# Optimization experiments

Measured on AMD Instinct MI355X. Metric: run time of the kernel, lower is better.

## Reference

```python
import jax, jax.numpy as jnp
import numpy as np

N = 65536      # points
C = 256        # channels
K = 16         # knn_samples
L = 4          # num_blocks
EXP = 4        # MLP expansion
EPS = 1e-5


def layer_norm(x, g, b):
    m = jnp.mean(x, axis=-1, keepdims=True)
    v = jnp.var(x, axis=-1, keepdims=True)
    return (x - m) * jax.lax.rsqrt(v + EPS) * g + b


def setup_inputs() -> dict:
    key = jax.random.key(0)
    ks = jax.random.split(key, 16)
    s = lambda fan_in: 1.0 / np.sqrt(fan_in)
    inp = {
        "x": jax.random.normal(ks[0], (N, C), jnp.float32),
        "knn_idx": jax.random.randint(ks[1], (N, K), 0, N, jnp.int32),
        # per-block stacked params (PyTorch Linear stored as [in, out] here)
        "ln1_g": jnp.ones((L, C), jnp.float32),
        "ln1_b": jnp.zeros((L, C), jnp.float32),
        "w_qkv": jax.random.uniform(ks[2], (L, C, 3 * C), jnp.float32, -s(C), s(C)),
        "w_proj": jax.random.uniform(ks[3], (L, C, C), jnp.float32, -s(C), s(C)),
        "b_proj": jax.random.uniform(ks[4], (L, C), jnp.float32, -s(C), s(C)),
        "ln2_g": jnp.ones((L, C), jnp.float32),
        "ln2_b": jnp.zeros((L, C), jnp.float32),
        "w_fc1": jax.random.uniform(ks[5], (L, C, EXP * C), jnp.float32, -s(C), s(C)),
        "b_fc1": jax.random.uniform(ks[6], (L, EXP * C), jnp.float32, -s(C), s(C)),
        "w_fc2": jax.random.uniform(ks[7], (L, EXP * C, C), jnp.float32, -s(EXP * C), s(EXP * C)),
        "b_fc2": jax.random.uniform(ks[8], (L, C), jnp.float32, -s(EXP * C), s(EXP * C)),
    }
    return inp


def reference(x, knn_idx, ln1_g, ln1_b, w_qkv, w_proj, b_proj,
              ln2_g, ln2_b, w_fc1, b_fc1, w_fc2, b_fc2):
    scale = C ** (-0.5)  # head_dim == C (num_heads == 1)
    for i in range(L):
        # --- KNN attention ---
        h = layer_norm(x, ln1_g[i], ln1_b[i])
        qkv = h @ w_qkv[i]                       # [N, 3C], no bias
        q, k, v = jnp.split(qkv, 3, axis=-1)     # each [N, C]
        kk = k[knn_idx]                          # [N, K, C] neighbor gather
        vv = v[knn_idx]                          # [N, K, C]
        scores = jnp.einsum('nc,nkc->nk', q, kk) * scale
        attn = jax.nn.softmax(scores, axis=-1)   # softmax over K neighbors
        out = jnp.einsum('nk,nkc->nc', attn, vv)
        x = x + (out @ w_proj[i] + b_proj[i])
        # --- MLP ---
        h2 = layer_norm(x, ln2_g[i], ln2_b[i])
        h2 = jax.nn.gelu(h2 @ w_fc1[i] + b_fc1[i], approximate=False)
        x = x + (h2 @ w_fc2[i] + b_fc2[i])
    return x
```

## Files before the change

### kernel.cpp

```cpp
#include <hip/hip_runtime.h>

typedef __attribute__((ext_vector_type(4))) float  f32x4;
typedef __attribute__((ext_vector_type(2))) float  f32x2;
typedef __attribute__((ext_vector_type(8))) __bf16 bf16x8;
typedef __attribute__((ext_vector_type(4))) short  s16x4;
typedef __attribute__((ext_vector_type(8))) short  s16x8;
typedef unsigned char uchar;

__device__ __forceinline__ unsigned short f2bf(float f) {
  unsigned u = __builtin_bit_cast(unsigned, f);
  u += 0x7FFFu + ((u >> 16) & 1u);
  return (unsigned short)(u >> 16);
}
__device__ __forceinline__ float b2f(short s) {
  return __builtin_bit_cast(float, (unsigned)((unsigned short)s) << 16);
}
__device__ __forceinline__ uchar f2fp8(float v) {
  return (uchar)(__builtin_amdgcn_cvt_pk_fp8_f32(v, v, 0, false) & 0xFF);
}
__device__ __forceinline__ float gelu_fast(float v) {
  float u = v * (0.7978845608f + 0.0356774081f * v * v);
  float t = __expf(-2.f * fabsf(u));
  float th = (1.f - t) / (1.f + t);
  th = (u >= 0.f) ? th : -th;
  return 0.5f * v * (1.f + th);
}

__device__ __forceinline__ void gload16(const void* g, void* l) {
  __builtin_amdgcn_global_load_lds(
      (const __attribute__((address_space(1))) void*)g,
      (__attribute__((address_space(3))) void*)l, 16, 0, 0);
}

__global__ __launch_bounds__(256) void wcast(const float* __restrict__ W,
                                             short* __restrict__ WT,
                                             int In, int Out) {
  int i = blockIdx.x * 256 + threadIdx.x;
  int lay = blockIdx.y;
  if (i >= In * Out) return;
  const float* w = W + (size_t)lay * In * Out;
  short* wt = WT + (size_t)lay * In * Out;
  int ii = i % In, oo = i / In;
  wt[(size_t)oo * In + ii] = (short)f2bf(w[(size_t)ii * Out + oo]);
}

__global__ __launch_bounds__(256) void ln_k(const float* __restrict__ x,
                                            const float* __restrict__ g,
                                            const float* __restrict__ b,
                                            short* __restrict__ out) {
  int row = blockIdx.x * 4 + (threadIdx.x >> 6);
  int l = threadIdx.x & 63;
  const float4 v = *(const float4*)(x + (size_t)row * 256 + l * 4);
  float s  = v.x + v.y + v.z + v.w;
  float ss = v.x * v.x + v.y * v.y + v.z * v.z + v.w * v.w;
#pragma unroll
  for (int o = 32; o >= 1; o >>= 1) {
    s  += __shfl_xor(s, o);
    ss += __shfl_xor(ss, o);
  }
  float mean = s * (1.0f / 256.0f);
  float var  = ss * (1.0f / 256.0f) - mean * mean;
  float rstd = rsqrtf(var + 1e-5f);
  const float4 gg = *(const float4*)(g + l * 4);
  const float4 bb = *(const float4*)(b + l * 4);
  s16x4 o4;
  o4[0] = (short)f2bf((v.x - mean) * rstd * gg.x + bb.x);
  o4[1] = (short)f2bf((v.y - mean) * rstd * gg.y + bb.y);
  o4[2] = (short)f2bf((v.z - mean) * rstd * gg.z + bb.z);
  o4[3] = (short)f2bf((v.w - mean) * rstd * gg.w + bb.w);
  *(s16x4*)(out + (size_t)row * 256 + l * 4) = o4;
}

__global__ __launch_bounds__(256) void attn_k(const short* __restrict__ q_,
                                              const uchar* __restrict__ k8,
                                              const uchar* __restrict__ v8,
                                              const int* __restrict__ knn,
                                              short* __restrict__ out) {
  int n = blockIdx.x * 4 + (threadIdx.x >> 6);
  int l = threadIdx.x & 63;
  int j = l & 15, g = l >> 4;
  int idxj = knn[(size_t)n * 16 + j];
  const short* qp = q_ + (size_t)n * 256 + g * 64;
  const uchar* kp = k8 + (size_t)idxj * 256 + g * 64;
  float partial = 0.f;
#pragma unroll
  for (int t = 0; t < 4; ++t) {
    int4 kv = *(const int4*)(kp + t * 16);
    s16x8 q0 = *(const s16x8*)(qp + t * 16);
    s16x8 q1 = *(const s16x8*)(qp + t * 16 + 8);
    f32x2 a;
    a = __builtin_amdgcn_cvt_pk_f32_fp8(kv.x, false);
    partial += a[0] * b2f(q0[0]) + a[1] * b2f(q0[1]);
    a = __builtin_amdgcn_cvt_pk_f32_fp8(kv.x, true);
    partial += a[0] * b2f(q0[2]) + a[1] * b2f(q0[3]);
    a = __builtin_amdgcn_cvt_pk_f32_fp8(kv.y, false);
    partial += a[0] * b2f(q0[4]) + a[1] * b2f(q0[5]);
    a = __builtin_amdgcn_cvt_pk_f32_fp8(kv.y, true);
    partial += a[0] * b2f(q0[6]) + a[1] * b2f(q0[7]);
    a = __builtin_amdgcn_cvt_pk_f32_fp8(kv.z, false);
    partial += a[0] * b2f(q1[0]) + a[1] * b2f(q1[1]);
    a = __builtin_amdgcn_cvt_pk_f32_fp8(kv.z, true);
    partial += a[0] * b2f(q1[2]) + a[1] * b2f(q1[3]);
    a = __builtin_amdgcn_cvt_pk_f32_fp8(kv.w, false);
    partial += a[0] * b2f(q1[4]) + a[1] * b2f(q1[5]);
    a = __builtin_amdgcn_cvt_pk_f32_fp8(kv.w, true);
    partial += a[0] * b2f(q1[6]) + a[1] * b2f(q1[7]);
  }
  partial += __shfl_xor(partial, 16);
  partial += __shfl_xor(partial, 32);
  float score = partial * 0.0625f;
  float mx = score;
#pragma unroll
  for (int o = 1; o < 16; o <<= 1) mx = fmaxf(mx, __shfl_xor(mx, o));
  float e = __expf(score - mx);
  float sum = e;
#pragma unroll
  for (int o = 1; o < 16; o <<= 1) sum += __shfl_xor(sum, o);
  float attn = e / sum;
  float4 o4 = {0.f, 0.f, 0.f, 0.f};
#pragma unroll
  for (int jj = 0; jj < 16; ++jj) {
    float aj = __shfl(attn, jj);
    int   ij = __shfl(idxj, jj);
    int vv = *(const int*)(v8 + (size_t)ij * 256 + l * 4);
    f32x2 lo = __builtin_amdgcn_cvt_pk_f32_fp8(vv, false);
    f32x2 hi = __builtin_amdgcn_cvt_pk_f32_fp8(vv, true);
    o4.x += aj * lo[0];
    o4.y += aj * lo[1];
    o4.z += aj * hi[0];
    o4.w += aj * hi[1];
  }
  s16x4 ob;
  ob[0] = (short)f2bf(o4.x);
  ob[1] = (short)f2bf(o4.y);
  ob[2] = (short)f2bf(o4.z);
  ob[3] = (short)f2bf(o4.w);
  *(s16x4*)(out + (size_t)n * 256 + l * 4) = ob;
}

template <int EPI, int KD>
__global__ __launch_bounds__(256) void gemm_k(
    const short* __restrict__ A, const short* __restrict__ BT,
    const float* __restrict__ bias, const float* __restrict__ resid,
    short* __restrict__ outb, float* __restrict__ outf,
    uchar* __restrict__ k8, uchar* __restrict__ v8, int Nout, int gx) {
  __shared__ __align__(16) char pool[36864];
  short* lA = (short*)pool;
  short* lB = (short*)(pool + 16384);
  const int tid = threadIdx.x;
  const int l = tid & 63, w = tid >> 6;
  const int nwg = gridDim.x;
  const int bid = blockIdx.x;
  const int swz = (bid & 7) * (nwg >> 3) + (bid >> 3);
  const int m0 = (swz / gx) << 7, n0 = (swz % gx) << 7;
  const int wm = w >> 1, wn = w & 1;

  f32x4 acc[4][4];
#pragma unroll
  for (int i = 0; i < 4; ++i)
#pragma unroll
    for (int jj = 0; jj < 4; ++jj) acc[i][jj] = f32x4{0.f, 0.f, 0.f, 0.f};

  const int srow = (w << 3) + (l >> 3);
  const int scol = (((l & 7) << 3)) ^ ((srow & 7) << 3);
  const short* gA = A + (size_t)(m0 + srow) * KD + scol;
  const short* gB = BT + (size_t)(n0 + srow) * KD + scol;

  for (int kt = 0; kt < KD; kt += 64) {
#pragma unroll
    for (int it = 0; it < 4; ++it) {
      gload16(gA + (size_t)(it * 32) * KD + kt, &lA[(it * 32 + w * 8) * 64]);
      gload16(gB + (size_t)(it * 32) * KD + kt, &lB[(it * 32 + w * 8) * 64]);
    }
    __syncthreads();
#pragma unroll
    for (int kc = 0; kc < 2; ++kc) {
      bf16x8 aF[4], bF[4];
#pragma unroll
      for (int f = 0; f < 4; ++f) {
        int r = wm * 64 + f * 16 + (l & 15);
        int ce = (kc * 32 + ((l >> 4) << 3)) ^ ((r & 7) << 3);
        aF[f] = *(const bf16x8*)(lA + r * 64 + ce);
      }
#pragma unroll
      for (int f = 0; f < 4; ++f) {
        int r = wn * 64 + f * 16 + (l & 15);
        int ce = (kc * 32 + ((l >> 4) << 3)) ^ ((r & 7) << 3);
        bF[f] = *(const bf16x8*)(lB + r * 64 + ce);
      }
#pragma unroll
      for (int mf = 0; mf < 4; ++mf)
#pragma unroll
        for (int nf = 0; nf < 4; ++nf)
          acc[mf][nf] = __builtin_amdgcn_mfma_f32_16x16x32_bf16(
              aF[mf], bF[nf], acc[mf][nf], 0, 0, 0);
    }
    __syncthreads();
  }

  const int lr = (l >> 4) << 2, lc = l & 15;
  if (EPI == 1) {
#pragma unroll
    for (int mf = 0; mf < 4; ++mf) {
#pragma unroll
      for (int nf = 0; nf < 4; ++nf) {
#pragma unroll
        for (int jj = 0; jj < 4; ++jj) {
          int row = m0 + wm * 64 + mf * 16 + lr + jj;
          int col = n0 + wn * 64 + nf * 16 + lc;
          float v = acc[mf][nf][jj] + bias[col] + resid[(size_t)row * 256 + col];
          outf[(size_t)row * 256 + col] = v;
        }
      }
    }
    return;
  }

  short* myL = (short*)(pool + w * 9216);
#pragma unroll
  for (int mf = 0; mf < 4; ++mf) {
#pragma unroll
    for (int nf = 0; nf < 4; ++nf) {
#pragma unroll
      for (int jj = 0; jj < 4; ++jj) {
        int rl = mf * 16 + lr + jj;
        int cl = nf * 16 + lc;
        float v = acc[mf][nf][jj];
        if (EPI == 2) v = gelu_fast(v + bias[n0 + wn * 64 + cl]);
        myL[rl * 72 + cl] = (short)f2bf(v);
      }
    }
  }
#pragma unroll
  for (int it = 0; it < 8; ++it) {
    int rl = it * 8 + (l >> 3);
    int cl = (l & 7) * 8;
    s16x8 vv = *(const s16x8*)(myL + rl * 72 + cl);
    int rowg = m0 + wm * 64 + rl;
    int colg = n0 + wn * 64 + cl;
    if (EPI == 2) {
      *(s16x8*)(outb + (size_t)rowg * Nout + colg) = vv;
    } else {
      if (colg < 256) {
        *(s16x8*)(outb + (size_t)rowg * 256 + colg) = vv;
      } else {
        unsigned w0 = __builtin_amdgcn_cvt_pk_fp8_f32(b2f(vv[0]), b2f(vv[1]), 0, false);
        w0 = __builtin_amdgcn_cvt_pk_fp8_f32(b2f(vv[2]), b2f(vv[3]), w0, true);
        unsigned w1 = __builtin_amdgcn_cvt_pk_fp8_f32(b2f(vv[4]), b2f(vv[5]), 0, false);
        w1 = __builtin_amdgcn_cvt_pk_fp8_f32(b2f(vv[6]), b2f(vv[7]), w1, true);
        int2 pk = make_int2((int)w0, (int)w1);
        uchar* dst = (colg < 512) ? (k8 + (size_t)rowg * 256 + (colg - 256))
                                  : (v8 + (size_t)rowg * 256 + (colg - 512));
        *(int2*)dst = pk;
      }
    }
  }
}

extern "C" void kernel_launch(void* const* d_in, const int* in_sizes, int n_in,
                              void* d_out, int out_size, void* d_ws, size_t ws_size,
                              hipStream_t stream) {
  const float* in_x   = (const float*)d_in[0];
  const int*   knn    = (const int*)d_in[1];
  const float* ln1_g  = (const float*)d_in[2];
  const float* ln1_b  = (const float*)d_in[3];
  const float* w_qkv  = (const float*)d_in[4];
  const float* w_proj = (const float*)d_in[5];
  const float* b_proj = (const float*)d_in[6];
  const float* ln2_g  = (const float*)d_in[7];
  const float* ln2_b  = (const float*)d_in[8];
  const float* w_fc1  = (const float*)d_in[9];
  const float* b_fc1  = (const float*)d_in[10];
  const float* w_fc2  = (const float*)d_in[11];
  const float* b_fc2  = (const float*)d_in[12];

  char* ws = (char*)d_ws;
  float* x    = (float*)(ws);
  short* act  = (short*)(ws + 67108864);
  short* big  = (short*)(ws + 100663296);
  short* q_bf = big;
  uchar* k8   = (uchar*)(ws + 134217728);
  uchar* v8   = (uchar*)(ws + 150994944);
  short* wT   = (short*)(ws + 234881024);
  short* wqkvT  = wT;
  short* wprojT = wT + 786432;
  short* wfc1T  = wT + 1048576;
  short* wfc2T  = wT + 2097152;

  wcast<<<dim3(768, 4), 256, 0, stream>>>(w_qkv, wqkvT, 256, 768);
  wcast<<<dim3(256, 4), 256, 0, stream>>>(w_proj, wprojT, 256, 256);
  wcast<<<dim3(1024, 4), 256, 0, stream>>>(w_fc1, wfc1T, 256, 1024);
  wcast<<<dim3(1024, 4), 256, 0, stream>>>(w_fc2, wfc2T, 1024, 256);

  for (int i = 0; i < 4; ++i) {
    const float* xin = (i == 0) ? in_x : x;
    ln_k<<<16384, 256, 0, stream>>>(xin, ln1_g + i * 256, ln1_b + i * 256, act);
    gemm_k<3, 256><<<3072, 256, 0, stream>>>(
        act, wqkvT + (size_t)i * 196608, nullptr, nullptr, q_bf, nullptr,
        k8, v8, 768, 6);
    attn_k<<<16384, 256, 0, stream>>>(q_bf, k8, v8, knn, act);
    gemm_k<1, 256><<<1024, 256, 0, stream>>>(
        act, wprojT + (size_t)i * 65536, b_proj + i * 256, xin, nullptr, x,
        nullptr, nullptr, 256, 2);
    ln_k<<<16384, 256, 0, stream>>>(x, ln2_g + i * 256, ln2_b + i * 256, act);
    gemm_k<2, 256><<<4096, 256, 0, stream>>>(
        act, wfc1T + (size_t)i * 262144, b_fc1 + i * 1024, nullptr, big, nullptr,
        nullptr, nullptr, 1024, 8);
    gemm_k<1, 1024><<<1024, 256, 0, stream>>>(
        big, wfc2T + (size_t)i * 262144, b_fc2 + i * 256, x, nullptr,
        (i == 3) ? (float*)d_out : x, nullptr, nullptr, 256, 2);
  }
}
```

Measured before the change: 1.268 ms.

## Quantize MLP hidden activations and fc2 weights to FP8 for fc2 GEMM

The fc1 epilogue now writes GELU outputs as scaled FP8 (×16) instead of bf16. fc2 weights are cast to FP8 (×64). A new FP8 MFMA GEMM kernel computes fc2 and rescales by 1/1024 before adding bias and the residual. This halves the bytes of the large hidden activation tensor and uses the faster FP8 matrix path, at the cost of extra quantization error in the MLP output.

New measurement: 1.248 ms. No clear change (-1.5%).

```diff
diff --git a/kernel.cpp b/kernel.cpp
--- a/kernel.cpp
+++ b/kernel.cpp
@@ -42,6 +42,16 @@
   short* wt = WT + (size_t)lay * In * Out;
   int ii = i % In, oo = i / In;
   wt[(size_t)oo * In + ii] = (short)f2bf(w[(size_t)ii * Out + oo]);
+}
+
+__global__ __launch_bounds__(256) void wcast8(const float* __restrict__ W,
+                                              uchar* __restrict__ WT8) {
+  int i = blockIdx.x * 256 + threadIdx.x;
+  int lay = blockIdx.y;
+  const float* w = W + (size_t)lay * 262144;
+  uchar* wt = WT8 + (size_t)lay * 262144;
+  int ii = i % 1024, oo = i / 1024;
+  wt[(size_t)oo * 1024 + ii] = f2fp8(64.f * w[(size_t)ii * 256 + oo]);
 }
 
 __global__ __launch_bounds__(256) void ln_k(const float* __restrict__ x,
@@ -239,7 +249,11 @@
     int rowg = m0 + wm * 64 + rl;
     int colg = n0 + wn * 64 + cl;
     if (EPI == 2) {
-      *(s16x8*)(outb + (size_t)rowg * Nout + colg) = vv;
+      unsigned w0 = __builtin_amdgcn_cvt_pk_fp8_f32(16.f * b2f(vv[0]), 16.f * b2f(vv[1]), 0, false);
+      w0 = __builtin_amdgcn_cvt_pk_fp8_f32(16.f * b2f(vv[2]), 16.f * b2f(vv[3]), w0, true);
+      unsigned w1 = __builtin_amdgcn_cvt_pk_fp8_f32(16.f * b2f(vv[4]), 16.f * b2f(vv[5]), 0, false);
+      w1 = __builtin_amdgcn_cvt_pk_fp8_f32(16.f * b2f(vv[6]), 16.f * b2f(vv[7]), w1, true);
+      *(int2*)(k8 + (size_t)rowg * Nout + colg) = make_int2((int)w0, (int)w1);
     } else {
       if (colg < 256) {
         *(s16x8*)(outb + (size_t)rowg * 256 + colg) = vv;
@@ -252,6 +266,80 @@
         uchar* dst = (colg < 512) ? (k8 + (size_t)rowg * 256 + (colg - 256))
                                   : (v8 + (size_t)rowg * 256 + (colg - 512));
         *(int2*)dst = pk;
+      }
+    }
+  }
+}
+
+__global__ __launch_bounds__(256) void gemm_fp8(
+    const uchar* __restrict__ A8, const uchar* __restrict__ B8,
+    const float* __restrict__ bias, const float* __restrict__ resid,
+    float* __restrict__ outf) {
+  __shared__ __align__(16) uchar lA8[8192];
+  __shared__ __align__(16) uchar lB8[8192];
+  const int tid = threadIdx.x;
+  const int l = tid & 63, w = tid >> 6;
+  const int nwg = gridDim.x;
+  const int bid = blockIdx.x;
+  const int swz = (bid & 7) * (nwg >> 3) + (bid >> 3);
+  const int m0 = (swz >> 1) << 7, n0 = (swz & 1) << 7;
+  const int wm = w >> 1, wn = w & 1;
+
+  f32x4 acc[4][4];
+#pragma unroll
+  for (int i = 0; i < 4; ++i)
+#pragma unroll
+    for (int jj = 0; jj < 4; ++jj) acc[i][jj] = f32x4{0.f, 0.f, 0.f, 0.f};
+
+  const int sr = (w << 4) + (l >> 2);
+  const int sc = ((l & 3) << 4) ^ ((sr & 3) << 4);
+  const uchar* gA = A8 + (size_t)(m0 + sr) * 1024 + sc;
+  const uchar* gB = B8 + (size_t)(n0 + sr) * 1024 + sc;
+
+  for (int kt = 0; kt < 1024; kt += 64) {
+#pragma unroll
+    for (int it = 0; it < 2; ++it) {
+      gload16(gA + (size_t)(it * 64) * 1024 + kt, &lA8[(it * 64 + w * 16) * 64]);
+      gload16(gB + (size_t)(it * 64) * 1024 + kt, &lB8[(it * 64 + w * 16) * 64]);
+    }
+    __syncthreads();
+#pragma unroll
+    for (int kc = 0; kc < 2; ++kc) {
+      long aF[4], bF[4];
+#pragma unroll
+      for (int f = 0; f < 4; ++f) {
+        int r = wm * 64 + f * 16 + (l & 15);
+        int cs = (kc * 32 + ((l >> 4) << 3)) ^ ((r & 3) << 4);
+        aF[f] = *(const long*)(lA8 + r * 64 + cs);
+      }
+#pragma unroll
+      for (int f = 0; f < 4; ++f) {
+        int r = wn * 64 + f * 16 + (l & 15);
+        int cs = (kc * 32 + ((l >> 4) << 3)) ^ ((r & 3) << 4);
+        bF[f] = *(const long*)(lB8 + r * 64 + cs);
+      }
+#pragma unroll
+      for (int mf = 0; mf < 4; ++mf)
+#pragma unroll
+        for (int nf = 0; nf < 4; ++nf)
+          acc[mf][nf] = __builtin_amdgcn_mfma_f32_16x16x32_fp8_fp8(
+              aF[mf], bF[nf], acc[mf][nf], 0, 0, 0);
+    }
+    __syncthreads();
+  }
+
+  const int lr = (l >> 4) << 2, lc = l & 15;
+#pragma unroll
+  for (int mf = 0; mf < 4; ++mf) {
+#pragma unroll
+    for (int nf = 0; nf < 4; ++nf) {
+#pragma unroll
+      for (int jj = 0; jj < 4; ++jj) {
+        int row = m0 + wm * 64 + mf * 16 + lr + jj;
+        int col = n0 + wn * 64 + nf * 16 + lc;
+        float v = acc[mf][nf][jj] * (1.0f / 1024.0f) + bias[col] +
+                  resid[(size_t)row * 256 + col];
+        outf[(size_t)row * 256 + col] = v;
       }
     }
   }
@@ -277,20 +365,20 @@
   char* ws = (char*)d_ws;
   float* x    = (float*)(ws);
   short* act  = (short*)(ws + 67108864);
-  short* big  = (short*)(ws + 100663296);
-  short* q_bf = big;
-  uchar* k8   = (uchar*)(ws + 134217728);
-  uchar* v8   = (uchar*)(ws + 150994944);
+  uchar* big8 = (uchar*)(ws + 100663296);
+  short* q_bf = (short*)(ws + 167772160);
+  uchar* k8   = (uchar*)(ws + 201326592);
+  uchar* v8   = (uchar*)(ws + 218103808);
   short* wT   = (short*)(ws + 234881024);
   short* wqkvT  = wT;
   short* wprojT = wT + 786432;
   short* wfc1T  = wT + 1048576;
-  short* wfc2T  = wT + 2097152;
+  uchar* wfc2T8 = (uchar*)(wT + 2097152);
 
   wcast<<<dim3(768, 4), 256, 0, stream>>>(w_qkv, wqkvT, 256, 768);
   wcast<<<dim3(256, 4), 256, 0, stream>>>(w_proj, wprojT, 256, 256);
   wcast<<<dim3(1024, 4), 256, 0, stream>>>(w_fc1, wfc1T, 256, 1024);
-  wcast<<<dim3(1024, 4), 256, 0, stream>>>(w_fc2, wfc2T, 1024, 256);
+  wcast8<<<dim3(1024, 4), 256, 0, stream>>>(w_fc2, wfc2T8);
 
   for (int i = 0; i < 4; ++i) {
     const float* xin = (i == 0) ? in_x : x;
@@ -304,10 +392,10 @@
         nullptr, nullptr, 256, 2);
     ln_k<<<16384, 256, 0, stream>>>(x, ln2_g + i * 256, ln2_b + i * 256, act);
     gemm_k<2, 256><<<4096, 256, 0, stream>>>(
-        act, wfc1T + (size_t)i * 262144, b_fc1 + i * 1024, nullptr, big, nullptr,
-        nullptr, nullptr, 1024, 8);
-    gemm_k<1, 1024><<<1024, 256, 0, stream>>>(
-        big, wfc2T + (size_t)i * 262144, b_fc2 + i * 256, x, nullptr,
-        (i == 3) ? (float*)d_out : x, nullptr, nullptr, 256, 2);
-  }
-}
+        act, wfc1T + (size_t)i * 262144, b_fc1 + i * 1024, nullptr, nullptr,
+        nullptr, big8, nullptr, 1024, 8);
+    gemm_fp8<<<1024, 256, 0, stream>>>(
+        big8, wfc2T8 + (size_t)i * 262144, b_fc2 + i * 256, x,
+        (i == 3) ? (float*)d_out : x);
+  }
+}
```

## Fuse MLP fc1+GELU+fc2 into single kernel keeping hidden activations on-chip

Applied to the files above, without the earlier changes.

Replaces the separate fc1 (with GELU epilogue) and fc2 GEMM launches with one kernel. Each workgroup takes 64 rows, computes the 1024-wide hidden layer in 128-column chunks, applies GELU into per-wave LDS, and accumulates fc2 directly in registers. This removes the round trip of the N×1024 bf16 hidden tensor through global memory. In exchange, weight fragments are read straight from global/L2 without LDS staging, and the fc2 accumulators raise register pressure, which can hurt occupancy.

After: 3.632 ms. +186.5%, slower.

```diff
diff --git a/kernel.cpp b/kernel.cpp
--- a/kernel.cpp
+++ b/kernel.cpp
@@ -14,9 +14,6 @@
 }
 __device__ __forceinline__ float b2f(short s) {
   return __builtin_bit_cast(float, (unsigned)((unsigned short)s) << 16);
-}
-__device__ __forceinline__ uchar f2fp8(float v) {
-  return (uchar)(__builtin_amdgcn_cvt_pk_fp8_f32(v, v, 0, false) & 0xFF);
 }
 __device__ __forceinline__ float gelu_fast(float v) {
   float u = v * (0.7978845608f + 0.0356774081f * v * v);
@@ -225,9 +222,7 @@
       for (int jj = 0; jj < 4; ++jj) {
         int rl = mf * 16 + lr + jj;
         int cl = nf * 16 + lc;
-        float v = acc[mf][nf][jj];
-        if (EPI == 2) v = gelu_fast(v + bias[n0 + wn * 64 + cl]);
-        myL[rl * 72 + cl] = (short)f2bf(v);
+        myL[rl * 72 + cl] = (short)f2bf(acc[mf][nf][jj]);
       }
     }
   }
@@ -238,21 +233,102 @@
     s16x8 vv = *(const s16x8*)(myL + rl * 72 + cl);
     int rowg = m0 + wm * 64 + rl;
     int colg = n0 + wn * 64 + cl;
-    if (EPI == 2) {
-      *(s16x8*)(outb + (size_t)rowg * Nout + colg) = vv;
+    if (colg < 256) {
+      *(s16x8*)(outb + (size_t)rowg * 256 + colg) = vv;
     } else {
-      if (colg < 256) {
-        *(s16x8*)(outb + (size_t)rowg * 256 + colg) = vv;
-      } else {
-        unsigned w0 = __builtin_amdgcn_cvt_pk_fp8_f32(b2f(vv[0]), b2f(vv[1]), 0, false);
-        w0 = __builtin_amdgcn_cvt_pk_fp8_f32(b2f(vv[2]), b2f(vv[3]), w0, true);
-        unsigned w1 = __builtin_amdgcn_cvt_pk_fp8_f32(b2f(vv[4]), b2f(vv[5]), 0, false);
-        w1 = __builtin_amdgcn_cvt_pk_fp8_f32(b2f(vv[6]), b2f(vv[7]), w1, true);
-        int2 pk = make_int2((int)w0, (int)w1);
-        uchar* dst = (colg < 512) ? (k8 + (size_t)rowg * 256 + (colg - 256))
-                                  : (v8 + (size_t)rowg * 256 + (colg - 512));
-        *(int2*)dst = pk;
-      }
+      unsigned w0 = __builtin_amdgcn_cvt_pk_fp8_f32(b2f(vv[0]), b2f(vv[1]), 0, false);
+      w0 = __builtin_amdgcn_cvt_pk_fp8_f32(b2f(vv[2]), b2f(vv[3]), w0, true);
+      unsigned w1 = __builtin_amdgcn_cvt_pk_fp8_f32(b2f(vv[4]), b2f(vv[5]), 0, false);
+      w1 = __builtin_amdgcn_cvt_pk_fp8_f32(b2f(vv[6]), b2f(vv[7]), w1, true);
+      int2 pk = make_int2((int)w0, (int)w1);
+      uchar* dst = (colg < 512) ? (k8 + (size_t)rowg * 256 + (colg - 256))
+                                : (v8 + (size_t)rowg * 256 + (colg - 512));
+      *(int2*)dst = pk;
+    }
+  }
+}
+
+__global__ __launch_bounds__(256) void mlp_k(
+    const short* __restrict__ act, const short* __restrict__ w1T,
+    const float* __restrict__ b1, const short* __restrict__ w2T,
+    const float* __restrict__ b2, const float* __restrict__ resid,
+    float* __restrict__ xout) {
+  __shared__ __align__(16) short lact[64 * 256];
+  __shared__ __align__(16) short la1[4][16 * 128];
+  const int tid = threadIdx.x;
+  const int l = tid & 63, w = tid >> 6;
+  const int nwg = gridDim.x;
+  const int bid = blockIdx.x;
+  const int swz = (bid & 7) * (nwg >> 3) + (bid >> 3);
+  const int m0 = swz << 6;
+
+  {
+    const int sr = w * 2 + (l >> 5);
+    const int sc = ((l & 31) << 3) ^ ((sr & 7) << 3);
+    const short* gA = act + (size_t)(m0 + sr) * 256 + sc;
+#pragma unroll
+    for (int it = 0; it < 8; ++it)
+      gload16(gA + (size_t)(it * 8) * 256, &lact[(it * 8 + w * 2) * 256]);
+  }
+  __syncthreads();
+
+  f32x4 acc2[16];
+#pragma unroll
+  for (int i = 0; i < 16; ++i) acc2[i] = f32x4{0.f, 0.f, 0.f, 0.f};
+
+  const int arow = w * 16 + (l & 15);
+  const int rxor = (l & 7) << 3;
+  const int lrr = ((l >> 4) << 2);
+
+  for (int nc = 0; nc < 8; ++nc) {
+    f32x4 acc1[8];
+#pragma unroll
+    for (int i = 0; i < 8; ++i) acc1[i] = f32x4{0.f, 0.f, 0.f, 0.f};
+#pragma unroll
+    for (int kc = 0; kc < 8; ++kc) {
+      int ce = (kc * 32 + ((l >> 4) << 3)) ^ rxor;
+      bf16x8 aF = *(const bf16x8*)(lact + arow * 256 + ce);
+      int wcol = kc * 32 + ((l >> 4) << 3);
+#pragma unroll
+      for (int nf = 0; nf < 8; ++nf) {
+        int wrow = nc * 128 + nf * 16 + (l & 15);
+        bf16x8 bF = *(const bf16x8*)(w1T + (size_t)wrow * 256 + wcol);
+        acc1[nf] = __builtin_amdgcn_mfma_f32_16x16x32_bf16(aF, bF, acc1[nf], 0, 0, 0);
+      }
+    }
+#pragma unroll
+    for (int nf = 0; nf < 8; ++nf) {
+#pragma unroll
+      for (int j = 0; j < 4; ++j) {
+        int colc = nf * 16 + (l & 15);
+        float v = gelu_fast(acc1[nf][j] + b1[nc * 128 + colc]);
+        int rr = lrr + j;
+        la1[w][rr * 128 + (colc ^ ((rr & 7) << 3))] = (short)f2bf(v);
+      }
+    }
+#pragma unroll
+    for (int kc = 0; kc < 4; ++kc) {
+      int rr = l & 15;
+      int ce = (kc * 32 + ((l >> 4) << 3)) ^ ((rr & 7) << 3);
+      bf16x8 aF = *(const bf16x8*)(&la1[w][rr * 128 + ce]);
+      int kcol = nc * 128 + kc * 32 + ((l >> 4) << 3);
+#pragma unroll
+      for (int nf = 0; nf < 16; ++nf) {
+        int orow = nf * 16 + (l & 15);
+        bf16x8 bF = *(const bf16x8*)(w2T + (size_t)orow * 1024 + kcol);
+        acc2[nf] = __builtin_amdgcn_mfma_f32_16x16x32_bf16(aF, bF, acc2[nf], 0, 0, 0);
+      }
+    }
+  }
+
+#pragma unroll
+  for (int nf = 0; nf < 16; ++nf) {
+#pragma unroll
+    for (int j = 0; j < 4; ++j) {
+      int row = m0 + w * 16 + lrr + j;
+      int col = nf * 16 + (l & 15);
+      float v = acc2[nf][j] + b2[col] + resid[(size_t)row * 256 + col];
+      xout[(size_t)row * 256 + col] = v;
     }
   }
 }
@@ -277,11 +353,10 @@
   char* ws = (char*)d_ws;
   float* x    = (float*)(ws);
   short* act  = (short*)(ws + 67108864);
-  short* big  = (short*)(ws + 100663296);
-  short* q_bf = big;
+  short* q_bf = (short*)(ws + 100663296);
   uchar* k8   = (uchar*)(ws + 134217728);
   uchar* v8   = (uchar*)(ws + 150994944);
-  short* wT   = (short*)(ws + 234881024);
+  short* wT   = (short*)(ws + 167772160);
   short* wqkvT  = wT;
   short* wprojT = wT + 786432;
   short* wfc1T  = wT + 1048576;
@@ -303,11 +378,9 @@
         act, wprojT + (size_t)i * 65536, b_proj + i * 256, xin, nullptr, x,
         nullptr, nullptr, 256, 2);
     ln_k<<<16384, 256, 0, stream>>>(x, ln2_g + i * 256, ln2_b + i * 256, act);
-    gemm_k<2, 256><<<4096, 256, 0, stream>>>(
-        act, wfc1T + (size_t)i * 262144, b_fc1 + i * 1024, nullptr, big, nullptr,
-        nullptr, nullptr, 1024, 8);
-    gemm_k<1, 1024><<<1024, 256, 0, stream>>>(
-        big, wfc2T + (size_t)i * 262144, b_fc2 + i * 256, x, nullptr,
-        (i == 3) ? (float*)d_out : x, nullptr, nullptr, 256, 2);
-  }
-}
+    mlp_k<<<1024, 256, 0, stream>>>(
+        act, wfc1T + (size_t)i * 262144, b_fc1 + i * 1024,
+        wfc2T + (size_t)i * 262144, b_fc2 + i * 256, x,
+        (i == 3) ? (float*)d_out : x);
+  }
+}
```

## Keep residual stream in bf16 and use sigmoid GELU approximation

Applied to the files above, without the earlier changes.

Stores the running residual x as bf16 instead of fp32, so layer norms and residual-add epilogues read and write half the bytes; an initial kernel casts the input to bf16 and the last block writes fp32 output. GELU in the fc1 epilogue is replaced by the cheaper x*sigmoid(1.702x) form. This cuts memory traffic and epilogue ALU work but accumulates rounding error in the residual across blocks and loosens GELU accuracy.

New measurement: 1.084 ms. 14.5% less time.

```diff
diff --git a/kernel.cpp b/kernel.cpp
--- a/kernel.cpp
+++ b/kernel.cpp
@@ -15,21 +15,27 @@
 __device__ __forceinline__ float b2f(short s) {
   return __builtin_bit_cast(float, (unsigned)((unsigned short)s) << 16);
 }
-__device__ __forceinline__ uchar f2fp8(float v) {
-  return (uchar)(__builtin_amdgcn_cvt_pk_fp8_f32(v, v, 0, false) & 0xFF);
-}
-__device__ __forceinline__ float gelu_fast(float v) {
-  float u = v * (0.7978845608f + 0.0356774081f * v * v);
-  float t = __expf(-2.f * fabsf(u));
-  float th = (1.f - t) / (1.f + t);
-  th = (u >= 0.f) ? th : -th;
-  return 0.5f * v * (1.f + th);
+__device__ __forceinline__ float gelu_sig(float v) {
+  float t = __expf(-1.702f * v);
+  return v * __builtin_amdgcn_rcpf(1.f + t);
 }
 
 __device__ __forceinline__ void gload16(const void* g, void* l) {
   __builtin_amdgcn_global_load_lds(
       (const __attribute__((address_space(1))) void*)g,
       (__attribute__((address_space(3))) void*)l, 16, 0, 0);
+}
+
+__global__ __launch_bounds__(256) void x2bf(const float* __restrict__ x,
+                                            short* __restrict__ xb) {
+  int i = blockIdx.x * 256 + threadIdx.x;
+  float4 v = *(const float4*)(x + (size_t)i * 4);
+  s16x4 o;
+  o[0] = (short)f2bf(v.x);
+  o[1] = (short)f2bf(v.y);
+  o[2] = (short)f2bf(v.z);
+  o[3] = (short)f2bf(v.w);
+  *(s16x4*)(xb + (size_t)i * 4) = o;
 }
 
 __global__ __launch_bounds__(256) void wcast(const float* __restrict__ W,
@@ -44,15 +50,16 @@
   wt[(size_t)oo * In + ii] = (short)f2bf(w[(size_t)ii * Out + oo]);
 }
 
-__global__ __launch_bounds__(256) void ln_k(const float* __restrict__ x,
+__global__ __launch_bounds__(256) void ln_k(const short* __restrict__ xb,
                                             const float* __restrict__ g,
                                             const float* __restrict__ b,
                                             short* __restrict__ out) {
   int row = blockIdx.x * 4 + (threadIdx.x >> 6);
   int l = threadIdx.x & 63;
-  const float4 v = *(const float4*)(x + (size_t)row * 256 + l * 4);
-  float s  = v.x + v.y + v.z + v.w;
-  float ss = v.x * v.x + v.y * v.y + v.z * v.z + v.w * v.w;
+  const s16x4 vb = *(const s16x4*)(xb + (size_t)row * 256 + l * 4);
+  float v0 = b2f(vb[0]), v1 = b2f(vb[1]), v2 = b2f(vb[2]), v3 = b2f(vb[3]);
+  float s  = v0 + v1 + v2 + v3;
+  float ss = v0 * v0 + v1 * v1 + v2 * v2 + v3 * v3;
 #pragma unroll
   for (int o = 32; o >= 1; o >>= 1) {
     s  += __shfl_xor(s, o);
@@ -64,10 +71,10 @@
   const float4 gg = *(const float4*)(g + l * 4);
   const float4 bb = *(const float4*)(b + l * 4);
   s16x4 o4;
-  o4[0] = (short)f2bf((v.x - mean) * rstd * gg.x + bb.x);
-  o4[1] = (short)f2bf((v.y - mean) * rstd * gg.y + bb.y);
-  o4[2] = (short)f2bf((v.z - mean) * rstd * gg.z + bb.z);
-  o4[3] = (short)f2bf((v.w - mean) * rstd * gg.w + bb.w);
+  o4[0] = (short)f2bf((v0 - mean) * rstd * gg.x + bb.x);
+  o4[1] = (short)f2bf((v1 - mean) * rstd * gg.y + bb.y);
+  o4[2] = (short)f2bf((v2 - mean) * rstd * gg.z + bb.z);
+  o4[3] = (short)f2bf((v3 - mean) * rstd * gg.w + bb.w);
   *(s16x4*)(out + (size_t)row * 256 + l * 4) = o4;
 }
 
@@ -141,7 +148,7 @@
 template <int EPI, int KD>
 __global__ __launch_bounds__(256) void gemm_k(
     const short* __restrict__ A, const short* __restrict__ BT,
-    const float* __restrict__ bias, const float* __restrict__ resid,
+    const float* __restrict__ bias, const short* __restrict__ residb,
     short* __restrict__ outb, float* __restrict__ outf,
     uchar* __restrict__ k8, uchar* __restrict__ v8, int Nout, int gx) {
   __shared__ __align__(16) char pool[36864];
@@ -199,7 +206,7 @@
   }
 
   const int lr = (l >> 4) << 2, lc = l & 15;
-  if (EPI == 1) {
+  if (EPI == 1 || EPI == 4) {
 #pragma unroll
     for (int mf = 0; mf < 4; ++mf) {
 #pragma unroll
@@ -208,8 +215,12 @@
         for (int jj = 0; jj < 4; ++jj) {
           int row = m0 + wm * 64 + mf * 16 + lr + jj;
           int col = n0 + wn * 64 + nf * 16 + lc;
-          float v = acc[mf][nf][jj] + bias[col] + resid[(size_t)row * 256 + col];
-          outf[(size_t)row * 256 + col] = v;
+          float v = acc[mf][nf][jj] + bias[col] +
+                    b2f(residb[(size_t)row * 256 + col]);
+          if (EPI == 1)
+            outb[(size_t)row * 256 + col] = (short)f2bf(v);
+          else
+            outf[(size_t)row * 256 + col] = v;
         }
       }
     }
@@ -226,7 +237,7 @@
         int rl = mf * 16 + lr + jj;
         int cl = nf * 16 + lc;
         float v = acc[mf][nf][jj];
-        if (EPI == 2) v = gelu_fast(v + bias[n0 + wn * 64 + cl]);
+        if (EPI == 2) v = gelu_sig(v + bias[n0 + wn * 64 + cl]);
         myL[rl * 72 + cl] = (short)f2bf(v);
       }
     }
@@ -275,39 +286,44 @@
   const float* b_fc2  = (const float*)d_in[12];
 
   char* ws = (char*)d_ws;
-  float* x    = (float*)(ws);
-  short* act  = (short*)(ws + 67108864);
-  short* big  = (short*)(ws + 100663296);
+  short* xb   = (short*)(ws);
+  short* act  = (short*)(ws + 33554432);
+  short* big  = (short*)(ws + 67108864);
   short* q_bf = big;
-  uchar* k8   = (uchar*)(ws + 134217728);
-  uchar* v8   = (uchar*)(ws + 150994944);
-  short* wT   = (short*)(ws + 234881024);
+  uchar* k8   = (uchar*)(ws + 100663296);
+  uchar* v8   = (uchar*)(ws + 117440512);
+  short* wT   = (short*)(ws + 201326592);
   short* wqkvT  = wT;
   short* wprojT = wT + 786432;
   short* wfc1T  = wT + 1048576;
   short* wfc2T  = wT + 2097152;
 
+  x2bf<<<16384, 256, 0, stream>>>(in_x, xb);
   wcast<<<dim3(768, 4), 256, 0, stream>>>(w_qkv, wqkvT, 256, 768);
   wcast<<<dim3(256, 4), 256, 0, stream>>>(w_proj, wprojT, 256, 256);
   wcast<<<dim3(1024, 4), 256, 0, stream>>>(w_fc1, wfc1T, 256, 1024);
   wcast<<<dim3(1024, 4), 256, 0, stream>>>(w_fc2, wfc2T, 1024, 256);
 
   for (int i = 0; i < 4; ++i) {
-    const float* xin = (i == 0) ? in_x : x;
-    ln_k<<<16384, 256, 0, stream>>>(xin, ln1_g + i * 256, ln1_b + i * 256, act);
+    ln_k<<<16384, 256, 0, stream>>>(xb, ln1_g + i * 256, ln1_b + i * 256, act);
     gemm_k<3, 256><<<3072, 256, 0, stream>>>(
         act, wqkvT + (size_t)i * 196608, nullptr, nullptr, q_bf, nullptr,
         k8, v8, 768, 6);
     attn_k<<<16384, 256, 0, stream>>>(q_bf, k8, v8, knn, act);
     gemm_k<1, 256><<<1024, 256, 0, stream>>>(
-        act, wprojT + (size_t)i * 65536, b_proj + i * 256, xin, nullptr, x,
-        nullptr, nullptr, 256, 2);
-    ln_k<<<16384, 256, 0, stream>>>(x, ln2_g + i * 256, ln2_b + i * 256, act);
+        act, wprojT + (size_t)i * 65536, b_proj + i * 256, xb, xb,
+        nullptr, nullptr, nullptr, 256, 2);
+    ln_k<<<16384, 256, 0, stream>>>(xb, ln2_g + i * 256, ln2_b + i * 256, act);
     gemm_k<2, 256><<<4096, 256, 0, stream>>>(
-        act, wfc1T + (size_t)i * 262144, b_fc1 + i * 1024, nullptr, big, nullptr,
-        nullptr, nullptr, 1024, 8);
-    gemm_k<1, 1024><<<1024, 256, 0, stream>>>(
-        big, wfc2T + (size_t)i * 262144, b_fc2 + i * 256, x, nullptr,
-        (i == 3) ? (float*)d_out : x, nullptr, nullptr, 256, 2);
-  }
-}
+        act, wfc1T + (size_t)i * 262144, b_fc1 + i * 1024, nullptr, big,
+        nullptr, nullptr, nullptr, 1024, 8);
+    if (i < 3)
+      gemm_k<1, 1024><<<1024, 256, 0, stream>>>(
+          big, wfc2T + (size_t)i * 262144, b_fc2 + i * 256, xb, xb,
+          nullptr, nullptr, nullptr, 256, 2);
+    else
+      gemm_k<4, 1024><<<1024, 256, 0, stream>>>(
+          big, wfc2T + (size_t)i * 262144, b_fc2 + i * 256, xb, nullptr,
+          (float*)d_out, nullptr, nullptr, 256, 2);
+  }
+}
```
